# Optimization experiments

Measured on AMD Instinct MI355X. Metric: run time of the kernel, lower is better.

## Reference

```python
import jax, jax.numpy as jnp
import numpy as np

N, NF, D, GH, E, B = 4096, 128, 64, 64, 32768, 32
NG, STEPS = 3, 3  # n_gcn, set2set processing steps


def setup_inputs() -> dict:
    key = jax.random.key(0)
    ks = iter(jax.random.split(key, 64))
    nrm = lambda shape: jax.random.normal(next(ks), shape, dtype=jnp.float32) * 0.05
    inp = {
        'x': jax.random.normal(next(ks), (N, NF), dtype=jnp.float32),
        'edge_attr': jax.random.uniform(next(ks), (E,), dtype=jnp.float32),
        'edge_idx': jax.random.randint(next(ks), (2, E), 0, N),
        'batch_map': jnp.sort(jax.random.randint(next(ks), (N,), 0, B)),
        # pre-GC MLP: NF->D, D->D, D->D (ReLU each)
        'pre_W0': nrm((NF, D)), 'pre_b0': nrm((D,)),
        'pre_W1': nrm((D, D)), 'pre_b1': nrm((D,)),
        'pre_W2': nrm((D, D)), 'pre_b2': nrm((D,)),
        # NNConv edge nets (stacked over NG layers): 1->GH->D*D
        'enn_W1': nrm((NG, 1, GH)), 'enn_b1': nrm((NG, GH)),
        'enn_W2': nrm((NG, GH, D * D)), 'enn_b2': nrm((NG, D * D)),
        'root_W': nrm((NG, D, D)), 'conv_b': nrm((NG, D)),
        # GRU(D, D) per layer, gate order r,z,n (torch), stored transposed for x@W
        'gru_Wih': nrm((NG, D, 3 * D)), 'gru_Whh': nrm((NG, D, 3 * D)),
        'gru_bih': nrm((NG, 3 * D)), 'gru_bhh': nrm((NG, 3 * D)),
        # Set2Set LSTM: input 2D -> hidden D, gate order i,f,g,o (torch)
        's2s_Wih': nrm((2 * D, 4 * D)), 's2s_Whh': nrm((D, 4 * D)),
        's2s_bih': nrm((4 * D,)), 's2s_bhh': nrm((4 * D,)),
        # post-GC MLP: 2D->D, D->D, D->D (ReLU each), then D->1
        'post_W0': nrm((2 * D, D)), 'post_b0': nrm((D,)),
        'post_W1': nrm((D, D)), 'post_b1': nrm((D,)),
        'post_W2': nrm((D, D)), 'post_b2': nrm((D,)),
        'post_W3': nrm((D, 1)), 'post_b3': nrm((1,)),
    }
    return inp


def _forward(x, edge_attr, pre_W0, pre_b0, pre_W1, pre_b1, pre_W2, pre_b2,
             enn_W1, enn_b1, enn_W2, enn_b2, root_W, conv_b,
             gru_Wih, gru_Whh, gru_bih, gru_bhh,
             s2s_Wih, s2s_Whh, s2s_bih, s2s_bhh,
             post_W0, post_b0, post_W1, post_b1, post_W2, post_b2,
             post_W3, post_b3, edge_idx, batch_map):
    relu, sig = jax.nn.relu, jax.nn.sigmoid
    # pre-GC layers
    out = relu(x @ pre_W0 + pre_b0)
    out = relu(out @ pre_W1 + pre_b1)
    out = relu(out @ pre_W2 + pre_b2)  # [N, D]

    src, dst = edge_idx[0], edge_idx[1]
    deg = jax.ops.segment_sum(jnp.ones((E,), out.dtype), dst, num_segments=N)
    deg = jnp.maximum(deg, 1.0)
    ea = edge_attr[:, None]  # view(-1, 1)

    for l in range(NG):
        h = out
        # NNConv: per-edge weight matrix from edge MLP
        We = relu(ea @ enn_W1[l] + enn_b1[l])              # [E, GH]
        We = (We @ enn_W2[l] + enn_b2[l]).reshape(E, D, D)  # [E, D, D]
        msg = jnp.einsum('ei,eio->eo', out[src], We)        # [E, D]
        agg = jax.ops.segment_sum(msg, dst, num_segments=N) / deg[:, None]
        conv = relu(agg + out @ root_W[l] + conv_b[l])
        # single-step GRU update (torch gate order r, z, n)
        gi = conv @ gru_Wih[l] + gru_bih[l]
        gh = h @ gru_Whh[l] + gru_bhh[l]
        i_r, i_z, i_n = jnp.split(gi, 3, axis=-1)
        h_r, h_z, h_n = jnp.split(gh, 3, axis=-1)
        r = sig(i_r + h_r)
        z = sig(i_z + h_z)
        n = jnp.tanh(i_n + r * h_n)
        out = (1.0 - z) * n + z * h

    # Set2Set pooling (early)
    q_star = jnp.zeros((B, 2 * D), out.dtype)
    hh = jnp.zeros((B, D), out.dtype)
    cc = jnp.zeros((B, D), out.dtype)
    for _ in range(STEPS):
        gates = q_star @ s2s_Wih + s2s_bih + hh @ s2s_Whh + s2s_bhh
        gi_, gf, gg, go = jnp.split(gates, 4, axis=-1)
        cc = sig(gf) * cc + sig(gi_) * jnp.tanh(gg)
        hh = sig(go) * jnp.tanh(cc)
        q = hh
        e = jnp.sum(out * q[batch_map], axis=-1)                    # [N]
        m = jax.ops.segment_max(e, batch_map, num_segments=B)
        a = jnp.exp(e - m[batch_map])
        den = jax.ops.segment_sum(a, batch_map, num_segments=B)
        a = a / den[batch_map]
        r_read = jax.ops.segment_sum(a[:, None] * out, batch_map, num_segments=B)
        q_star = jnp.concatenate([q, r_read], axis=-1)              # [B, 2D]

    # post-GC layers
    y = relu(q_star @ post_W0 + post_b0)
    y = relu(y @ post_W1 + post_b1)
    y = relu(y @ post_W2 + post_b2)
    y = y @ post_W3 + post_b3  # [B, 1]
    return y


def reference(x, edge_attr, edge_idx, batch_map, pre_W0, pre_b0, pre_W1, pre_b1,
              pre_W2, pre_b2, enn_W1, enn_b1, enn_W2, enn_b2, root_W, conv_b,
              gru_Wih, gru_Whh, gru_bih, gru_bhh, s2s_Wih, s2s_Whh, s2s_bih,
              s2s_bhh, post_W0, post_b0, post_W1, post_b1, post_W2, post_b2,
              post_W3, post_b3):
    return _forward(x, edge_attr, pre_W0, pre_b0, pre_W1, pre_b1, pre_W2, pre_b2,
                    enn_W1, enn_b1, enn_W2, enn_b2, root_W, conv_b,
                    gru_Wih, gru_Whh, gru_bih, gru_bhh,
                    s2s_Wih, s2s_Whh, s2s_bih, s2s_bhh,
                    post_W0, post_b0, post_W1, post_b1, post_W2, post_b2,
                    post_W3, post_b3, edge_idx, batch_map)
```

## Files before the change

### kernel.cpp

```cpp
#include <hip/hip_runtime.h>
#include <hip/hip_bf16.h>
#include <string.h>

#define NN   4096
#define NE   32768
#define NB   32
#define BKT  64
#define MSG_CHUNK 8

typedef __attribute__((ext_vector_type(8))) short short8;
typedef __attribute__((ext_vector_type(4))) float f4;

__device__ __forceinline__ float sigf(float x) { return 1.0f / (1.0f + __expf(-x)); }
__device__ __forceinline__ short f2bf(float f) {
    __hip_bfloat16 h = __float2bfloat16(f);
    short s;
    memcpy(&s, &h, sizeof(short));
    return s;
}

__global__ __launch_bounds__(256) void k_setup(const float* __restrict__ x,
        const float* __restrict__ W0, const float* __restrict__ b0,
        const float* __restrict__ W1, const float* __restrict__ b1,
        const float* __restrict__ W2, const float* __restrict__ b2,
        const float* __restrict__ enn_W2, __hip_bfloat16* __restrict__ W2F,
        float* __restrict__ out, float* __restrict__ agg,
        int* cnt_src, int* cnt_dst, int* bstart, int* bend) {
    int bid = blockIdx.x, t = threadIdx.x;
    if (bid < 32) {
        int i = bid * 256 + t;
        if (i < NN) cnt_src[i] = 0;
        else cnt_dst[i - NN] = 0;
        if (i < NB) { bstart[i] = 0x7FFFFFFF; bend[i] = 0; }
    } else if (bid < 224) {
        __shared__ __hip_bfloat16 tile[4096];
        size_t base = (size_t)(bid - 32) * 4096;
        for (int i = t; i < 4096; i += 256) {
            int k = i >> 6, o = i & 63;
            int pos = ((o >> 4) << 10) | ((k >> 5) << 9) | (((k >> 3) & 3) << 7)
                    | ((o & 15) << 3) | (k & 7);
            tile[pos] = __float2bfloat16(enn_W2[base + i]);
        }
        __syncthreads();
        for (int i = t; i < 4096; i += 256) W2F[base + i] = tile[i];
    } else {
        __shared__ float xr[4][128], ha[4][64], hb[4][64];
        int w = t >> 6, j = t & 63;
        int n = (bid - 224) * 4 + w;
        xr[w][j] = x[(size_t)n * 128 + j];
        xr[w][64 + j] = x[(size_t)n * 128 + 64 + j];
        agg[(size_t)n * 64 + j] = 0.f;
        float s = b0[j];
        #pragma unroll 8
        for (int k = 0; k < 128; ++k) s = fmaf(xr[w][k], W0[k * 64 + j], s);
        ha[w][j] = fmaxf(s, 0.f);
        s = b1[j];
        #pragma unroll 8
        for (int k = 0; k < 64; ++k) s = fmaf(ha[w][k], W1[k * 64 + j], s);
        hb[w][j] = fmaxf(s, 0.f);
        s = b2[j];
        #pragma unroll 8
        for (int k = 0; k < 64; ++k) s = fmaf(hb[w][k], W2[k * 64 + j], s);
        out[(size_t)n * 64 + j] = fmaxf(s, 0.f);
    }
}

__global__ __launch_bounds__(256) void k_bucket(const int* __restrict__ eidx,
        const float* __restrict__ ea, const int* __restrict__ bm,
        const float* __restrict__ Wih, const float* __restrict__ Whh,
        float* __restrict__ WihT, float* __restrict__ WhhT,
        int* cnt_src, int* cnt_dst, int* csr_dst, float* csr_ea,
        int* bstart, int* bend) {
    int t = threadIdx.x;
    if (blockIdx.x >= 128) {
        int c0 = (blockIdx.x - 128) * 8;
        for (int i = t; i < 1024; i += 256) {
            int c = c0 + (i >> 7), j = i & 127;
            WihT[(size_t)c * 128 + j] = Wih[(size_t)j * 256 + c];
        }
        for (int i = t; i < 512; i += 256) {
            int c = c0 + (i >> 6), j = i & 63;
            WhhT[(size_t)c * 64 + j] = Whh[(size_t)j * 256 + c];
        }
        return;
    }
    int e = blockIdx.x * 256 + t;
    if (e < NE) {
        int s = eidx[e];
        int d = eidx[NE + e];
        int slot = atomicAdd(&cnt_src[s], 1);
        if (slot < BKT) {
            csr_dst[s * BKT + slot] = d;
            csr_ea[s * BKT + slot] = ea[e];
        }
        atomicAdd(&cnt_dst[d], 1);
    }
    if (e < NN) {
        int b = bm[e];
        atomicMin(&bstart[b], e);
        atomicMax(&bend[b], e + 1);
    }
}

__global__ __launch_bounds__(256, 2) void k_fused(const float* __restrict__ out,
        const __hip_bfloat16* __restrict__ W2F_l, const float* __restrict__ b2l,
        const float* __restrict__ W1l, const float* __restrict__ b1l,
        const int* __restrict__ cnt_src, const int* __restrict__ csr_dst,
        const float* __restrict__ csr_ea, float* __restrict__ agg) {
    __shared__ __hip_bfloat16 Pt[8 * 4096];
    __shared__ float outs[8][68];
    __shared__ float wlds[4][MSG_CHUNK][64];
    int t = threadIdx.x, wave = t >> 6, lane = t & 63;
    int laneM = lane & 15, quad = lane >> 4;
    int n0 = blockIdx.x * 8;
    for (int i = t; i < 512; i += 256) outs[i >> 6][i & 63] = out[(size_t)n0 * 64 + i];
    __syncthreads();
    short8 a0, a1;
    {
        const float* ar = &outs[laneM & 7][quad * 8];
        #pragma unroll
        for (int j = 0; j < 8; ++j) a0[j] = f2bf(ar[j]);
        const float* ar2 = &outs[laneM & 7][32 + quad * 8];
        #pragma unroll
        for (int j = 0; j < 8; ++j) a1[j] = f2bf(ar2[j]);
    }
    float btr[2] = {0.f, 0.f};
    for (int k = 0; k < 64; ++k) {
        float bv = b2l[k * 64 + lane];
        #pragma unroll
        for (int u = 0; u < 2; ++u) btr[u] = fmaf(outs[wave * 2 + u][k], bv, btr[u]);
    }
    #pragma unroll 2
    for (int gp = 0; gp < 8; ++gp) {
        int gA = wave * 16 + gp * 2;
        const __hip_bfloat16* BgA = W2F_l + (size_t)gA * 4096;
        const __hip_bfloat16* BgB = BgA + 4096;
        int c = gA >> 3;
        int p = (gA >> 1) & 3;
        char* wb = (char*)Pt + (quad << 15) + (c << 10) + (laneM << 4)
                 + (((p ^ quad) & 3) << 2);
        #pragma unroll
        for (int sub = 0; sub < 4; ++sub) {
            short8 bA0 = *(const short8*)(BgA + sub * 1024 + lane * 8);
            short8 bA1 = *(const short8*)(BgA + sub * 1024 + 512 + lane * 8);
            short8 bB0 = *(const short8*)(BgB + sub * 1024 + lane * 8);
            short8 bB1 = *(const short8*)(BgB + sub * 1024 + 512 + lane * 8);
            f4 accA = {0.f, 0.f, 0.f, 0.f}, accB = {0.f, 0.f, 0.f, 0.f};
            accA = __builtin_amdgcn_mfma_f32_16x16x32_bf16(a0, bA0, accA, 0, 0, 0);
            accA = __builtin_amdgcn_mfma_f32_16x16x32_bf16(a1, bA1, accA, 0, 0, 0);
            accB = __builtin_amdgcn_mfma_f32_16x16x32_bf16(a0, bB0, accB, 0, 0, 0);
            accB = __builtin_amdgcn_mfma_f32_16x16x32_bf16(a1, bB1, accB, 0, 0, 0);
            if (quad < 2) {
                char* wbs = wb + (sub << 8);
                #pragma unroll
                for (int r = 0; r < 4; ++r) {
                    unsigned pk = (unsigned)(unsigned short)f2bf(accA[r])
                                | ((unsigned)(unsigned short)f2bf(accB[r]) << 16);
                    *(unsigned*)(wbs + (r << 13)) = pk;
                }
            }
        }
    }
    __syncthreads();
    float w1v = W1l[lane], b1v = b1l[lane];
    for (int u = 0; u < 2; ++u) {
        int nloc = wave * 2 + u;
        int n = n0 + nloc;
        int deg = cnt_src[n];
        if (deg > BKT) deg = BKT;
        if (deg <= 0) continue;
        int wq = nloc >> 2;
        float preg[64];
        const char* Pn = (const char*)Pt + (nloc << 13);
        #pragma unroll
        for (int c = 0; c < 8; ++c) {
            uint4 vv = *(const uint4*)(Pn + (c << 10) + (lane << 4));
            unsigned d0 = vv.x, d1 = vv.y, d2 = vv.z, d3 = vv.w;
            if (wq & 1) { unsigned tt = d0; d0 = d1; d1 = tt; tt = d2; d2 = d3; d3 = tt; }
            union { unsigned u2; float f; } cv;
            cv.u2 = d0 << 16;          preg[c * 8 + 0] = cv.f;
            cv.u2 = d0 & 0xFFFF0000u;  preg[c * 8 + 1] = cv.f;
            cv.u2 = d1 << 16;          preg[c * 8 + 2] = cv.f;
            cv.u2 = d1 & 0xFFFF0000u;  preg[c * 8 + 3] = cv.f;
            cv.u2 = d2 << 16;          preg[c * 8 + 4] = cv.f;
            cv.u2 = d2 & 0xFFFF0000u;  preg[c * 8 + 5] = cv.f;
            cv.u2 = d3 << 16;          preg[c * 8 + 6] = cv.f;
            cv.u2 = d3 & 0xFFFF0000u;  preg[c * 8 + 7] = cv.f;
        }
        float bt = btr[u];
        const int* bdst = csr_dst + n * BKT;
        const float* bea = csr_ea + n * BKT;
        for (int c0 = 0; c0 < deg; c0 += MSG_CHUNK) {
            int cc = deg - c0;
            if (cc > MSG_CHUNK) cc = MSG_CHUNK;
            int dl = 0; float el = 0.f;
            if (lane < cc) { dl = bdst[c0 + lane]; el = bea[c0 + lane]; }
            for (int si = 0; si < cc; ++si) {
                float eav = __shfl(el, si, 64);
                wlds[wave][si][lane] = fmaxf(fmaf(eav, w1v, b1v), 0.f);
            }
            for (int i = 0; i < cc; ++i) {
                int dst = __shfl(dl, i, 64);
                const float* wr = wlds[wave][i];
                float acc0 = bt, acc1 = 0.f, acc2 = 0.f, acc3 = 0.f;
                #pragma unroll
                for (int g = 0; g < 64; g += 16) {
                    float4 w0 = *(const float4*)(wr + g);
                    float4 w1 = *(const float4*)(wr + g + 4);
                    float4 w2 = *(const float4*)(wr + g + 8);
                    float4 w3 = *(const float4*)(wr + g + 12);
                    acc0 = fmaf(w0.x, preg[g], acc0);
                    acc0 = fmaf(w0.y, preg[g + 1], acc0);
                    acc0 = fmaf(w0.z, preg[g + 2], acc0);
                    acc0 = fmaf(w0.w, preg[g + 3], acc0);
                    acc1 = fmaf(w1.x, preg[g + 4], acc1);
                    acc1 = fmaf(w1.y, preg[g + 5], acc1);
                    acc1 = fmaf(w1.z, preg[g + 6], acc1);
                    acc1 = fmaf(w1.w, preg[g + 7], acc1);
                    acc2 = fmaf(w2.x, preg[g + 8], acc2);
                    acc2 = fmaf(w2.y, preg[g + 9], acc2);
                    acc2 = fmaf(w2.z, preg[g + 10], acc2);
                    acc2 = fmaf(w2.w, preg[g + 11], acc2);
                    acc3 = fmaf(w3.x, preg[g + 12], acc3);
                    acc3 = fmaf(w3.y, preg[g + 13], acc3);
                    acc3 = fmaf(w3.z, preg[g + 14], acc3);
                    acc3 = fmaf(w3.w, preg[g + 15], acc3);
                }
                float acc = (acc0 + acc1) + (acc2 + acc3);
                atomicAdd(&agg[(size_t)dst * 64 + lane], acc);
            }
        }
    }
}

__global__ __launch_bounds__(256) void k_gru(const float* __restrict__ out,
        float* __restrict__ agg, const int* __restrict__ cnt_dst,
        const float* __restrict__ rootW, const float* __restrict__ convb,
        const float* __restrict__ Wih, const float* __restrict__ Whh,
        const float* __restrict__ bih, const float* __restrict__ bhh,
        float* __restrict__ outn) {
    __shared__ float sh[4][64], sc[4][64];
    int t = threadIdx.x, w = t >> 6, j = t & 63;
    int n = blockIdx.x * 4 + w;
    float hj = out[(size_t)n * 64 + j];
    sh[w][j] = hj;
    int dg = cnt_dst[n];
    float invd = 1.0f / (float)(dg > 0 ? dg : 1);
    float av = agg[(size_t)n * 64 + j];
    agg[(size_t)n * 64 + j] = 0.f;
    __syncthreads();
    float s = av * invd + convb[j];
    #pragma unroll 8
    for (int k = 0; k < 64; ++k) s = fmaf(sh[w][k], rootW[k * 64 + j], s);
    float conv = fmaxf(s, 0.f);
    sc[w][j] = conv;
    __syncthreads();
    float gir = bih[j], giz = bih[64 + j], gin = bih[128 + j];
    float ghr = bhh[j], ghz = bhh[64 + j], ghn = bhh[128 + j];
    #pragma unroll 4
    for (int k = 0; k < 64; ++k) {
        float c = sc[w][k], h = sh[w][k];
        gir = fmaf(c, Wih[k * 192 + j], gir);
        giz = fmaf(c, Wih[k * 192 + 64 + j], giz);
        gin = fmaf(c, Wih[k * 192 + 128 + j], gin);
        ghr = fmaf(h, Whh[k * 192 + j], ghr);
        ghz = fmaf(h, Whh[k * 192 + 64 + j], ghz);
        ghn = fmaf(h, Whh[k * 192 + 128 + j], ghn);
    }
    float r = sigf(gir + ghr);
    float z = sigf(giz + ghz);
    float nn = tanhf(gin + r * ghn);
    outn[(size_t)n * 64 + j] = (1.f - z) * nn + z * hj;
}

__global__ __launch_bounds__(256, 1) void k_s2s_post(const float* __restrict__ out,
        const int* __restrict__ bstart, const int* __restrict__ bend,
        const float* __restrict__ WihT, const float* __restrict__ WhhT,
        const float* __restrict__ bih, const float* __restrict__ bhh,
        const float* __restrict__ pW0, const float* __restrict__ pb0,
        const float* __restrict__ pW1, const float* __restrict__ pb1,
        const float* __restrict__ pW2, const float* __restrict__ pb2,
        const float* __restrict__ pW3, const float* __restrict__ pb3,
        float* __restrict__ y) {
    __shared__ float cacheT[64 * 193];
    __shared__ float wpost[16448];
    __shared__ float qs[128];
    __shared__ float hh_l[64];
    __shared__ float gates_l[256];
    __shared__ float ebuf[1024];
    __shared__ float redw[4], redw2[4];
    __shared__ float redbuf[4][64];
    __shared__ float tmp64[64];
    int t = threadIdx.x, wave = t >> 6, lane = t & 63;
    int b = blockIdx.x;
    int s0 = bstart[b], e0 = bend[b];
    int cnt = e0 - s0;
    if (cnt < 0) cnt = 0;
    if (cnt > 1024) cnt = 1024;
    int ccnt = cnt < 192 ? cnt : 192;
    int nf4 = ccnt * 16;
    const float4* out4 = (const float4*)(out + (size_t)s0 * 64);
    float4 stg[12];
    #pragma unroll
    for (int i = 0; i < 12; ++i) {
        int v = t + i * 256;
        if (v < nf4) stg[i] = out4[v];
    }
    #pragma unroll
    for (int i = 0; i < 12; ++i) {
        int v = t + i * 256;
        if (v < nf4) {
            int row = v >> 4, dq = v & 15;
            cacheT[(dq * 4 + 0) * 193 + row] = stg[i].x;
            cacheT[(dq * 4 + 1) * 193 + row] = stg[i].y;
            cacheT[(dq * 4 + 2) * 193 + row] = stg[i].z;
            cacheT[(dq * 4 + 3) * 193 + row] = stg[i].w;
        }
    }
    {
        float4* wp4 = (float4*)wpost;
        #pragma unroll
        for (int i = 0; i < 8; ++i) {
            int v = t + i * 256;
            wp4[v] = ((const float4*)pW0)[v];
        }
        #pragma unroll
        for (int i = 0; i < 4; ++i) {
            int v = t + i * 256;
            wp4[2048 + v] = ((const float4*)pW1)[v];
        }
        #pragma unroll
        for (int i = 0; i < 4; ++i) {
            int v = t + i * 256;
            wp4[3072 + v] = ((const float4*)pW2)[v];
        }
        if (t < 16) wp4[4096 + t] = ((const float4*)pW3)[t];
    }
    const float4* wihT4 = (const float4*)(WihT + (size_t)t * 128);
    const float4* whhT4 = (const float4*)(WhhT + (size_t)t * 64);
    float bsum = bih[t] + bhh[t];
    float ccr = 0.f;
    if (t < 128) qs[t] = 0.f;
    if (t < 64) hh_l[t] = 0.f;
    __syncthreads();
    const float4* qs4 = (const float4*)qs;
    const float4* hh4 = (const float4*)hh_l;
    for (int step = 0; step < 3; ++step) {
        float g0 = bsum, g1 = 0.f, g2 = 0.f, g3 = 0.f;
        #pragma unroll
        for (int jq = 0; jq < 32; ++jq) {
            float4 w = wihT4[jq];
            float4 v = qs4[jq];
            g0 = fmaf(v.x, w.x, g0);
            g1 = fmaf(v.y, w.y, g1);
            g2 = fmaf(v.z, w.z, g2);
            g3 = fmaf(v.w, w.w, g3);
        }
        #pragma unroll
        for (int jq = 0; jq < 16; ++jq) {
            float4 w = whhT4[jq];
            float4 v = hh4[jq];
            g0 = fmaf(v.x, w.x, g0);
            g1 = fmaf(v.y, w.y, g1);
            g2 = fmaf(v.z, w.z, g2);
            g3 = fmaf(v.w, w.w, g3);
        }
        gates_l[t] = (g0 + g1) + (g2 + g3);
        __syncthreads();
        if (t < 64) {
            float cn = sigf(gates_l[64 + t]) * ccr
                     + sigf(gates_l[t]) * tanhf(gates_l[128 + t]);
            ccr = cn;
            hh_l[t] = sigf(gates_l[192 + t]) * tanhf(cn);
        }
        __syncthreads();
        for (int idx = t; idx < cnt; idx += 256) {
            float s0a = 0.f, s1a = 0.f, s2a = 0.f, s3a = 0.f;
            if (idx < 192) {
                #pragma unroll
                for (int dq = 0; dq < 16; ++dq) {
                    float4 h = hh4[dq];
                    s0a = fmaf(cacheT[(dq * 4 + 0) * 193 + idx], h.x, s0a);
                    s1a = fmaf(cacheT[(dq * 4 + 1) * 193 + idx], h.y, s1a);
                    s2a = fmaf(cacheT[(dq * 4 + 2) * 193 + idx], h.z, s2a);
                    s3a = fmaf(cacheT[(dq * 4 + 3) * 193 + idx], h.w, s3a);
                }
            } else {
                const float* row = out + (size_t)(s0 + idx) * 64;
                #pragma unroll
                for (int dq = 0; dq < 16; ++dq) {
                    float4 h = hh4[dq];
                    s0a = fmaf(row[dq * 4 + 0], h.x, s0a);
                    s1a = fmaf(row[dq * 4 + 1], h.y, s1a);
                    s2a = fmaf(row[dq * 4 + 2], h.z, s2a);
                    s3a = fmaf(row[dq * 4 + 3], h.w, s3a);
                }
            }
            ebuf[idx] = (s0a + s1a) + (s2a + s3a);
        }
        __syncthreads();
        float lm = -3.0e38f;
        for (int idx = t; idx < cnt; idx += 256) lm = fmaxf(lm, ebuf[idx]);
        #pragma unroll
        for (int off = 32; off > 0; off >>= 1) lm = fmaxf(lm, __shfl_xor(lm, off, 64));
        if (lane == 0) redw[wave] = lm;
        __syncthreads();
        float m = fmaxf(fmaxf(redw[0], redw[1]), fmaxf(redw[2], redw[3]));
        float ls = 0.f;
        for (int idx = t; idx < cnt; idx += 256) {
            float a = __expf(ebuf[idx] - m);
            ebuf[idx] = a;
            ls += a;
        }
        #pragma unroll
        for (int off = 32; off > 0; off >>= 1) ls += __shfl_xor(ls, off, 64);
        if (lane == 0) redw2[wave] = ls;
        __syncthreads();
        float ssum = (redw2[0] + redw2[1]) + (redw2[2] + redw2[3]);
        float inv = (cnt > 0) ? 1.f / ssum : 0.f;
        float r0 = 0.f;
        for (int row = wave; row < ccnt; row += 4)
            r0 = fmaf(ebuf[row], cacheT[lane * 193 + row], r0);
        for (int row = 192 + wave; row < cnt; row += 4)
            r0 = fmaf(ebuf[row], out[(size_t)(s0 + row) * 64 + lane], r0);
        redbuf[wave][lane] = r0;
        __syncthreads();
        if (t < 64) {
            float s = ((redbuf[0][t] + redbuf[1][t]) + (redbuf[2][t] + redbuf[3][t]));
            qs[64 + t] = s * inv;
            qs[t] = hh_l[t];
        }
        __syncthreads();
    }
    if (t < 64) {
        float s = pb0[t];
        #pragma unroll 4
        for (int k = 0; k < 128; ++k) s = fmaf(qs[k], wpost[k * 64 + t], s);
        tmp64[t] = fmaxf(s, 0.f);
    }
    __syncthreads();
    float h1v = 0.f;
    if (t < 64) {
        float s = pb1[t];
        #pragma unroll 4
        for (int k = 0; k < 64; ++k) s = fmaf(tmp64[k], wpost[8192 + k * 64 + t], s);
        h1v = fmaxf(s, 0.f);
    }
    __syncthreads();
    if (t < 64) tmp64[t] = h1v;
    __syncthreads();
    if (t < 64) {
        float s = pb2[t];
        #pragma unroll 4
        for (int k = 0; k < 64; ++k) s = fmaf(tmp64[k], wpost[12288 + k * 64 + t], s);
        gates_l[t] = fmaxf(s, 0.f) * wpost[16384 + t];
    }
    __syncthreads();
    if (t == 0) {
        float yy = pb3[0];
        for (int k = 0; k < 64; ++k) yy += gates_l[k];
        y[b] = yy;
    }
}


extern "C" void kernel_launch(void* const* d_in, const int* in_sizes, int n_in,
                              void* d_out, int out_size, void* d_ws, size_t ws_size,
                              hipStream_t stream) {
    const float* x         = (const float*)d_in[0];
    const float* edge_attr = (const float*)d_in[1];
    const int*   edge_idx  = (const int*)d_in[2];
    const int*   batch_map = (const int*)d_in[3];
    const float* pre_W0 = (const float*)d_in[4];
    const float* pre_b0 = (const float*)d_in[5];
    const float* pre_W1 = (const float*)d_in[6];
    const float* pre_b1 = (const float*)d_in[7];
    const float* pre_W2 = (const float*)d_in[8];
    const float* pre_b2 = (const float*)d_in[9];
    const float* enn_W1 = (const float*)d_in[10];
    const float* enn_b1 = (const float*)d_in[11];
    const float* enn_W2 = (const float*)d_in[12];
    const float* enn_b2 = (const float*)d_in[13];
    const float* root_W = (const float*)d_in[14];
    const float* conv_b = (const float*)d_in[15];
    const float* gru_Wih = (const float*)d_in[16];
    const float* gru_Whh = (const float*)d_in[17];
    const float* gru_bih = (const float*)d_in[18];
    const float* gru_bhh = (const float*)d_in[19];
    const float* s2s_Wih = (const float*)d_in[20];
    const float* s2s_Whh = (const float*)d_in[21];
    const float* s2s_bih = (const float*)d_in[22];
    const float* s2s_bhh = (const float*)d_in[23];
    const float* post_W0 = (const float*)d_in[24];
    const float* post_b0 = (const float*)d_in[25];
    const float* post_W1 = (const float*)d_in[26];
    const float* post_b1 = (const float*)d_in[27];
    const float* post_W2 = (const float*)d_in[28];
    const float* post_b2 = (const float*)d_in[29];
    const float* post_W3 = (const float*)d_in[30];
    const float* post_b3 = (const float*)d_in[31];
    float* yout = (float*)d_out;

    char* wp = (char*)d_ws;
    auto take = [&](size_t bytes) -> char* {
        char* r = wp;
        wp += (bytes + 255) & ~(size_t)255;
        return r;
    };
    float* outA = (float*)take((size_t)NN * 64 * 4);
    float* outB = (float*)take((size_t)NN * 64 * 4);
    float* agg  = (float*)take((size_t)NN * 64 * 4);
    __hip_bfloat16* W2F = (__hip_bfloat16*)take((size_t)3 * 64 * 4096 * 2);
    int* cnt_src  = (int*)take((size_t)NN * 4);
    int* cnt_dst  = (int*)take((size_t)NN * 4);
    int* csr_dst  = (int*)take((size_t)NN * BKT * 4);
    float* csr_ea = (float*)take((size_t)NN * BKT * 4);
    int* bstart   = (int*)take((size_t)NB * 4);
    int* bend     = (int*)take((size_t)NB * 4);
    float* WihT   = (float*)take((size_t)256 * 128 * 4);
    float* WhhT   = (float*)take((size_t)256 * 64 * 4);

    k_setup<<<1248, 256, 0, stream>>>(x, pre_W0, pre_b0, pre_W1, pre_b1, pre_W2, pre_b2,
                                      enn_W2, W2F, outA, agg, cnt_src, cnt_dst,
                                      bstart, bend);
    k_bucket<<<160, 256, 0, stream>>>(edge_idx, edge_attr, batch_map,
                                      s2s_Wih, s2s_Whh, WihT, WhhT,
                                      cnt_src, cnt_dst, csr_dst, csr_ea, bstart, bend);

    float* cur = outA;
    float* nxt = outB;
    for (int l = 0; l < 3; ++l) {
        k_fused<<<NN / 8, 256, 0, stream>>>(cur, W2F + (size_t)l * 64 * 4096,
                                            enn_b2 + (size_t)l * 4096,
                                            enn_W1 + l * 64, enn_b1 + l * 64,
                                            cnt_src, csr_dst, csr_ea, agg);
        k_gru<<<NN / 4, 256, 0, stream>>>(cur, agg, cnt_dst, root_W + l * 4096,
                                          conv_b + l * 64, gru_Wih + l * 64 * 192,
                                          gru_Whh + l * 64 * 192, gru_bih + l * 192,
                                          gru_bhh + l * 192, nxt);
        float* tmp = cur; cur = nxt; nxt = tmp;
    }
    k_s2s_post<<<NB, 256, 0, stream>>>(cur, bstart, bend, WihT, WhhT, s2s_bih,
                                       s2s_bhh, post_W0, post_b0, post_W1, post_b1,
                                       post_W2, post_b2, post_W3, post_b3, yout);
}
```

Baseline: 348.8 us.

## Fuse pre-MLP, NNConv message passing and GRU layers into one cooperative kernel

Replaces the per-layer k_fused/k_gru launches and the pre-MLP stage with a single cooperative persistent kernel of 512 blocks. Each block keeps its 8 node states in shared memory across all three layers and uses grid.sync between the scatter and GRU phases. This removes six kernel launches and the global round-trips of node features between layers. The cost is grid-wide barriers, a requirement that all 512 blocks be co-resident, and atomicExch to read and reset the aggregate buffer.

```diff
diff --git a/kernel.cpp b/kernel.cpp
--- a/kernel.cpp
+++ b/kernel.cpp
@@ -1,6 +1,9 @@
 #include <hip/hip_runtime.h>
 #include <hip/hip_bf16.h>
+#include <hip/hip_cooperative_groups.h>
 #include <string.h>
+
+namespace cg = cooperative_groups;
 
 #define NN   4096
 #define NE   32768
@@ -19,12 +22,8 @@
     return s;
 }
 
-__global__ __launch_bounds__(256) void k_setup(const float* __restrict__ x,
-        const float* __restrict__ W0, const float* __restrict__ b0,
-        const float* __restrict__ W1, const float* __restrict__ b1,
-        const float* __restrict__ W2, const float* __restrict__ b2,
-        const float* __restrict__ enn_W2, __hip_bfloat16* __restrict__ W2F,
-        float* __restrict__ out, float* __restrict__ agg,
+__global__ __launch_bounds__(256) void k_setup(const float* __restrict__ enn_W2,
+        __hip_bfloat16* __restrict__ W2F, float* __restrict__ agg,
         int* cnt_src, int* cnt_dst, int* bstart, int* bend) {
     int bid = blockIdx.x, t = threadIdx.x;
     if (bid < 32) {
@@ -32,7 +31,8 @@
         if (i < NN) cnt_src[i] = 0;
         else cnt_dst[i - NN] = 0;
         if (i < NB) { bstart[i] = 0x7FFFFFFF; bend[i] = 0; }
-    } else if (bid < 224) {
+        for (int z = i; z < NN * 64; z += 8192) agg[z] = 0.f;
+    } else {
         __shared__ __hip_bfloat16 tile[4096];
         size_t base = (size_t)(bid - 32) * 4096;
         for (int i = t; i < 4096; i += 256) {
@@ -43,25 +43,6 @@
         }
         __syncthreads();
         for (int i = t; i < 4096; i += 256) W2F[base + i] = tile[i];
-    } else {
-        __shared__ float xr[4][128], ha[4][64], hb[4][64];
-        int w = t >> 6, j = t & 63;
-        int n = (bid - 224) * 4 + w;
-        xr[w][j] = x[(size_t)n * 128 + j];
-        xr[w][64 + j] = x[(size_t)n * 128 + 64 + j];
-        agg[(size_t)n * 64 + j] = 0.f;
-        float s = b0[j];
-        #pragma unroll 8
-        for (int k = 0; k < 128; ++k) s = fmaf(xr[w][k], W0[k * 64 + j], s);
-        ha[w][j] = fmaxf(s, 0.f);
-        s = b1[j];
-        #pragma unroll 8
-        for (int k = 0; k < 64; ++k) s = fmaf(ha[w][k], W1[k * 64 + j], s);
-        hb[w][j] = fmaxf(s, 0.f);
-        s = b2[j];
-        #pragma unroll 8
-        for (int k = 0; k < 64; ++k) s = fmaf(hb[w][k], W2[k * 64 + j], s);
-        out[(size_t)n * 64 + j] = fmaxf(s, 0.f);
     }
 }
 
@@ -102,175 +83,218 @@
     }
 }
 
-__global__ __launch_bounds__(256, 2) void k_fused(const float* __restrict__ out,
-        const __hip_bfloat16* __restrict__ W2F_l, const float* __restrict__ b2l,
-        const float* __restrict__ W1l, const float* __restrict__ b1l,
-        const int* __restrict__ cnt_src, const int* __restrict__ csr_dst,
-        const float* __restrict__ csr_ea, float* __restrict__ agg) {
+__global__ __launch_bounds__(256, 2) void k_mega(const float* __restrict__ x,
+        const float* __restrict__ mW0, const float* __restrict__ mb0,
+        const float* __restrict__ mW1, const float* __restrict__ mb1,
+        const float* __restrict__ mW2, const float* __restrict__ mb2,
+        const __hip_bfloat16* __restrict__ W2F, const float* __restrict__ enn_b2,
+        const float* __restrict__ enn_W1, const float* __restrict__ enn_b1,
+        const float* __restrict__ rootW, const float* __restrict__ convb,
+        const float* __restrict__ gWih, const float* __restrict__ gWhh,
+        const float* __restrict__ gbih, const float* __restrict__ gbhh,
+        const int* __restrict__ cnt_src, const int* __restrict__ cnt_dst,
+        const int* __restrict__ csr_dst, const float* __restrict__ csr_ea,
+        float* __restrict__ agg, float* __restrict__ outG) {
+    cg::grid_group grid = cg::this_grid();
+    __shared__ float outs[8][68];
     __shared__ __hip_bfloat16 Pt[8 * 4096];
-    __shared__ float outs[8][68];
     __shared__ float wlds[4][MSG_CHUNK][64];
     int t = threadIdx.x, wave = t >> 6, lane = t & 63;
     int laneM = lane & 15, quad = lane >> 4;
     int n0 = blockIdx.x * 8;
-    for (int i = t; i < 512; i += 256) outs[i >> 6][i & 63] = out[(size_t)n0 * 64 + i];
-    __syncthreads();
-    short8 a0, a1;
-    {
-        const float* ar = &outs[laneM & 7][quad * 8];
-        #pragma unroll
-        for (int j = 0; j < 8; ++j) a0[j] = f2bf(ar[j]);
-        const float* ar2 = &outs[laneM & 7][32 + quad * 8];
-        #pragma unroll
-        for (int j = 0; j < 8; ++j) a1[j] = f2bf(ar2[j]);
-    }
-    float btr[2] = {0.f, 0.f};
-    for (int k = 0; k < 64; ++k) {
-        float bv = b2l[k * 64 + lane];
-        #pragma unroll
-        for (int u = 0; u < 2; ++u) btr[u] = fmaf(outs[wave * 2 + u][k], bv, btr[u]);
-    }
-    #pragma unroll 2
-    for (int gp = 0; gp < 8; ++gp) {
-        int gA = wave * 16 + gp * 2;
-        const __hip_bfloat16* BgA = W2F_l + (size_t)gA * 4096;
-        const __hip_bfloat16* BgB = BgA + 4096;
-        int c = gA >> 3;
-        int p = (gA >> 1) & 3;
-        char* wb = (char*)Pt + (quad << 15) + (c << 10) + (laneM << 4)
-                 + (((p ^ quad) & 3) << 2);
-        #pragma unroll
-        for (int sub = 0; sub < 4; ++sub) {
-            short8 bA0 = *(const short8*)(BgA + sub * 1024 + lane * 8);
-            short8 bA1 = *(const short8*)(BgA + sub * 1024 + 512 + lane * 8);
-            short8 bB0 = *(const short8*)(BgB + sub * 1024 + lane * 8);
-            short8 bB1 = *(const short8*)(BgB + sub * 1024 + 512 + lane * 8);
-            f4 accA = {0.f, 0.f, 0.f, 0.f}, accB = {0.f, 0.f, 0.f, 0.f};
-            accA = __builtin_amdgcn_mfma_f32_16x16x32_bf16(a0, bA0, accA, 0, 0, 0);
-            accA = __builtin_amdgcn_mfma_f32_16x16x32_bf16(a1, bA1, accA, 0, 0, 0);
-            accB = __builtin_amdgcn_mfma_f32_16x16x32_bf16(a0, bB0, accB, 0, 0, 0);
-            accB = __builtin_amdgcn_mfma_f32_16x16x32_bf16(a1, bB1, accB, 0, 0, 0);
-            if (quad < 2) {
-                char* wbs = wb + (sub << 8);
-                #pragma unroll
-                for (int r = 0; r < 4; ++r) {
-                    unsigned pk = (unsigned)(unsigned short)f2bf(accA[r])
-                                | ((unsigned)(unsigned short)f2bf(accB[r]) << 16);
-                    *(unsigned*)(wbs + (r << 13)) = pk;
+    int j = lane;
+    float* xs  = (float*)Pt;
+    float* haL = &wlds[0][0][0];
+    float* hbL = haL + 512;
+    for (int i = t; i < 1024; i += 256) xs[i] = x[(size_t)n0 * 128 + i];
+    __syncthreads();
+    for (int u = 0; u < 2; ++u) {
+        int nl = wave * 2 + u;
+        const float* xr = xs + nl * 128;
+        float s = mb0[j];
+        #pragma unroll 8
+        for (int k = 0; k < 128; ++k) s = fmaf(xr[k], mW0[k * 64 + j], s);
+        haL[nl * 64 + j] = fmaxf(s, 0.f);
+        s = mb1[j];
+        #pragma unroll 8
+        for (int k = 0; k < 64; ++k) s = fmaf(haL[nl * 64 + k], mW1[k * 64 + j], s);
+        hbL[nl * 64 + j] = fmaxf(s, 0.f);
+        s = mb2[j];
+        #pragma unroll 8
+        for (int k = 0; k < 64; ++k) s = fmaf(hbL[nl * 64 + k], mW2[k * 64 + j], s);
+        outs[nl][j] = fmaxf(s, 0.f);
+    }
+    __syncthreads();
+    for (int l = 0; l < 3; ++l) {
+        const __hip_bfloat16* W2F_l = W2F + (size_t)l * 64 * 4096;
+        const float* b2l = enn_b2 + (size_t)l * 4096;
+        const float* W1l = enn_W1 + l * 64;
+        const float* b1l = enn_b1 + l * 64;
+        short8 a0, a1;
+        {
+            const float* ar = &outs[laneM & 7][quad * 8];
+            #pragma unroll
+            for (int q = 0; q < 8; ++q) a0[q] = f2bf(ar[q]);
+            const float* ar2 = &outs[laneM & 7][32 + quad * 8];
+            #pragma unroll
+            for (int q = 0; q < 8; ++q) a1[q] = f2bf(ar2[q]);
+        }
+        float btr[2] = {0.f, 0.f};
+        for (int k = 0; k < 64; ++k) {
+            float bv = b2l[k * 64 + lane];
+            #pragma unroll
+            for (int u = 0; u < 2; ++u) btr[u] = fmaf(outs[wave * 2 + u][k], bv, btr[u]);
+        }
+        #pragma unroll 2
+        for (int gp = 0; gp < 8; ++gp) {
+            int gA = wave * 16 + gp * 2;
+            const __hip_bfloat16* BgA = W2F_l + (size_t)gA * 4096;
+            const __hip_bfloat16* BgB = BgA + 4096;
+            int c = gA >> 3;
+            int p = (gA >> 1) & 3;
+            char* wb = (char*)Pt + (quad << 15) + (c << 10) + (laneM << 4)
+                     + (((p ^ quad) & 3) << 2);
+            #pragma unroll
+            for (int sub = 0; sub < 4; ++sub) {
+                short8 bA0 = *(const short8*)(BgA + sub * 1024 + lane * 8);
+                short8 bA1 = *(const short8*)(BgA + sub * 1024 + 512 + lane * 8);
+                short8 bB0 = *(const short8*)(BgB + sub * 1024 + lane * 8);
+                short8 bB1 = *(const short8*)(BgB + sub * 1024 + 512 + lane * 8);
+                f4 accA = {0.f, 0.f, 0.f, 0.f}, accB = {0.f, 0.f, 0.f, 0.f};
+                accA = __builtin_amdgcn_mfma_f32_16x16x32_bf16(a0, bA0, accA, 0, 0, 0);
+                accA = __builtin_amdgcn_mfma_f32_16x16x32_bf16(a1, bA1, accA, 0, 0, 0);
+                accB = __builtin_amdgcn_mfma_f32_16x16x32_bf16(a0, bB0, accB, 0, 0, 0);
+                accB = __builtin_amdgcn_mfma_f32_16x16x32_bf16(a1, bB1, accB, 0, 0, 0);
+                if (quad < 2) {
+                    char* wbs = wb + (sub << 8);
+                    #pragma unroll
+                    for (int r = 0; r < 4; ++r) {
+                        unsigned pk = (unsigned)(unsigned short)f2bf(accA[r])
+                                    | ((unsigned)(unsigned short)f2bf(accB[r]) << 16);
+                        *(unsigned*)(wbs + (r << 13)) = pk;
+                    }
                 }
             }
         }
-    }
-    __syncthreads();
-    float w1v = W1l[lane], b1v = b1l[lane];
-    for (int u = 0; u < 2; ++u) {
-        int nloc = wave * 2 + u;
-        int n = n0 + nloc;
-        int deg = cnt_src[n];
-        if (deg > BKT) deg = BKT;
-        if (deg <= 0) continue;
-        int wq = nloc >> 2;
-        float preg[64];
-        const char* Pn = (const char*)Pt + (nloc << 13);
-        #pragma unroll
-        for (int c = 0; c < 8; ++c) {
-            uint4 vv = *(const uint4*)(Pn + (c << 10) + (lane << 4));
-            unsigned d0 = vv.x, d1 = vv.y, d2 = vv.z, d3 = vv.w;
-            if (wq & 1) { unsigned tt = d0; d0 = d1; d1 = tt; tt = d2; d2 = d3; d3 = tt; }
-            union { unsigned u2; float f; } cv;
-            cv.u2 = d0 << 16;          preg[c * 8 + 0] = cv.f;
-            cv.u2 = d0 & 0xFFFF0000u;  preg[c * 8 + 1] = cv.f;
-            cv.u2 = d1 << 16;          preg[c * 8 + 2] = cv.f;
-            cv.u2 = d1 & 0xFFFF0000u;  preg[c * 8 + 3] = cv.f;
-            cv.u2 = d2 << 16;          preg[c * 8 + 4] = cv.f;
-            cv.u2 = d2 & 0xFFFF0000u;  preg[c * 8 + 5] = cv.f;
-            cv.u2 = d3 << 16;          preg[c * 8 + 6] = cv.f;
-            cv.u2 = d3 & 0xFFFF0000u;  preg[c * 8 + 7] = cv.f;
-        }
-        float bt = btr[u];
-        const int* bdst = csr_dst + n * BKT;
-        const float* bea = csr_ea + n * BKT;
-        for (int c0 = 0; c0 < deg; c0 += MSG_CHUNK) {
-            int cc = deg - c0;
-            if (cc > MSG_CHUNK) cc = MSG_CHUNK;
-            int dl = 0; float el = 0.f;
-            if (lane < cc) { dl = bdst[c0 + lane]; el = bea[c0 + lane]; }
-            for (int si = 0; si < cc; ++si) {
-                float eav = __shfl(el, si, 64);
-                wlds[wave][si][lane] = fmaxf(fmaf(eav, w1v, b1v), 0.f);
+        __syncthreads();
+        float w1v = W1l[lane], b1v = b1l[lane];
+        for (int u = 0; u < 2; ++u) {
+            int nloc = wave * 2 + u;
+            int n = n0 + nloc;
+            int deg = cnt_src[n];
+            if (deg > BKT) deg = BKT;
+            if (deg <= 0) continue;
+            int wq = nloc >> 2;
+            float preg[64];
+            const char* Pn = (const char*)Pt + (nloc << 13);
+            #pragma unroll
+            for (int c = 0; c < 8; ++c) {
+                uint4 vv = *(const uint4*)(Pn + (c << 10) + (lane << 4));
+                unsigned d0 = vv.x, d1 = vv.y, d2 = vv.z, d3 = vv.w;
+                if (wq & 1) { unsigned tt = d0; d0 = d1; d1 = tt; tt = d2; d2 = d3; d3 = tt; }
+                union { unsigned u2; float f; } cv;
+                cv.u2 = d0 << 16;          preg[c * 8 + 0] = cv.f;
+                cv.u2 = d0 & 0xFFFF0000u;  preg[c * 8 + 1] = cv.f;
+                cv.u2 = d1 << 16;          preg[c * 8 + 2] = cv.f;
+                cv.u2 = d1 & 0xFFFF0000u;  preg[c * 8 + 3] = cv.f;
+                cv.u2 = d2 << 16;          preg[c * 8 + 4] = cv.f;
+                cv.u2 = d2 & 0xFFFF0000u;  preg[c * 8 + 5] = cv.f;
+                cv.u2 = d3 << 16;          preg[c * 8 + 6] = cv.f;
+                cv.u2 = d3 & 0xFFFF0000u;  preg[c * 8 + 7] = cv.f;
             }
-            for (int i = 0; i < cc; ++i) {
-                int dst = __shfl(dl, i, 64);
-                const float* wr = wlds[wave][i];
-                float acc0 = bt, acc1 = 0.f, acc2 = 0.f, acc3 = 0.f;
-                #pragma unroll
-                for (int g = 0; g < 64; g += 16) {
-                    float4 w0 = *(const float4*)(wr + g);
-                    float4 w1 = *(const float4*)(wr + g + 4);
-                    float4 w2 = *(const float4*)(wr + g + 8);
-                    float4 w3 = *(const float4*)(wr + g + 12);
-                    acc0 = fmaf(w0.x, preg[g], acc0);
-                    acc0 = fmaf(w0.y, preg[g + 1], acc0);
-                    acc0 = fmaf(w0.z, preg[g + 2], acc0);
-                    acc0 = fmaf(w0.w, preg[g + 3], acc0);
-                    acc1 = fmaf(w1.x, preg[g + 4], acc1);
-                    acc1 = fmaf(w1.y, preg[g + 5], acc1);
-                    acc1 = fmaf(w1.z, preg[g + 6], acc1);
-                    acc1 = fmaf(w1.w, preg[g + 7], acc1);
-                    acc2 = fmaf(w2.x, preg[g + 8], acc2);
-                    acc2 = fmaf(w2.y, preg[g + 9], acc2);
-                    acc2 = fmaf(w2.z, preg[g + 10], acc2);
-                    acc2 = fmaf(w2.w, preg[g + 11], acc2);
-                    acc3 = fmaf(w3.x, preg[g + 12], acc3);
-                    acc3 = fmaf(w3.y, preg[g + 13], acc3);
-                    acc3 = fmaf(w3.z, preg[g + 14], acc3);
-                    acc3 = fmaf(w3.w, preg[g + 15], acc3);
+            float bt = btr[u];
+            const int* bdst = csr_dst + n * BKT;
+            const float* bea = csr_ea + n * BKT;
+            for (int c0 = 0; c0 < deg; c0 += MSG_CHUNK) {
+                int cc = deg - c0;
+                if (cc > MSG_CHUNK) cc = MSG_CHUNK;
+                int dl = 0; float el = 0.f;
+                if (lane < cc) { dl = bdst[c0 + lane]; el = bea[c0 + lane]; }
+                for (int si = 0; si < cc; ++si) {
+                    float eav = __shfl(el, si, 64);
+                    wlds[wave][si][lane] = fmaxf(fmaf(eav, w1v, b1v), 0.f);
                 }
-                float acc = (acc0 + acc1) + (acc2 + acc3);
-                atomicAdd(&agg[(size_t)dst * 64 + lane], acc);
+                for (int i = 0; i < cc; ++i) {
+                    int dst = __shfl(dl, i, 64);
+                    const float* wr = wlds[wave][i];
+                    float acc0 = bt, acc1 = 0.f, acc2 = 0.f, acc3 = 0.f;
+                    #pragma unroll
+                    for (int g = 0; g < 64; g += 16) {
+                        float4 w0 = *(const float4*)(wr + g);
+                        float4 w1 = *(const float4*)(wr + g + 4);
+                        float4 w2 = *(const float4*)(wr + g + 8);
+                        float4 w3 = *(const float4*)(wr + g + 12);
+                        acc0 = fmaf(w0.x, preg[g], acc0);
+                        acc0 = fmaf(w0.y, preg[g + 1], acc0);
+                        acc0 = fmaf(w0.z, preg[g + 2], acc0);
+                        acc0 = fmaf(w0.w, preg[g + 3], acc0);
+                        acc1 = fmaf(w1.x, preg[g + 4], acc1);
+                        acc1 = fmaf(w1.y, preg[g + 5], acc1);
+                        acc1 = fmaf(w1.z, preg[g + 6], acc1);
+                        acc1 = fmaf(w1.w, preg[g + 7], acc1);
+                        acc2 = fmaf(w2.x, preg[g + 8], acc2);
+                        acc2 = fmaf(w2.y, preg[g + 9], acc2);
+                        acc2 = fmaf(w2.z, preg[g + 10], acc2);
+                        acc2 = fmaf(w2.w, preg[g + 11], acc2);
+                        acc3 = fmaf(w3.x, preg[g + 12], acc3);
+                        acc3 = fmaf(w3.y, preg[g + 13], acc3);
+                        acc3 = fmaf(w3.z, preg[g + 14], acc3);
+                        acc3 = fmaf(w3.w, preg[g + 15], acc3);
+                    }
+                    float acc = (acc0 + acc1) + (acc2 + acc3);
+                    atomicAdd(&agg[(size_t)dst * 64 + lane], acc);
+                }
             }
         }
-    }
-}
-
-__global__ __launch_bounds__(256) void k_gru(const float* __restrict__ out,
-        float* __restrict__ agg, const int* __restrict__ cnt_dst,
-        const float* __restrict__ rootW, const float* __restrict__ convb,
-        const float* __restrict__ Wih, const float* __restrict__ Whh,
-        const float* __restrict__ bih, const float* __restrict__ bhh,
-        float* __restrict__ outn) {
-    __shared__ float sh[4][64], sc[4][64];
-    int t = threadIdx.x, w = t >> 6, j = t & 63;
-    int n = blockIdx.x * 4 + w;
-    float hj = out[(size_t)n * 64 + j];
-    sh[w][j] = hj;
-    int dg = cnt_dst[n];
-    float invd = 1.0f / (float)(dg > 0 ? dg : 1);
-    float av = agg[(size_t)n * 64 + j];
-    agg[(size_t)n * 64 + j] = 0.f;
-    __syncthreads();
-    float s = av * invd + convb[j];
-    #pragma unroll 8
-    for (int k = 0; k < 64; ++k) s = fmaf(sh[w][k], rootW[k * 64 + j], s);
-    float conv = fmaxf(s, 0.f);
-    sc[w][j] = conv;
-    __syncthreads();
-    float gir = bih[j], giz = bih[64 + j], gin = bih[128 + j];
-    float ghr = bhh[j], ghz = bhh[64 + j], ghn = bhh[128 + j];
-    #pragma unroll 4
-    for (int k = 0; k < 64; ++k) {
-        float c = sc[w][k], h = sh[w][k];
-        gir = fmaf(c, Wih[k * 192 + j], gir);
-        giz = fmaf(c, Wih[k * 192 + 64 + j], giz);
-        gin = fmaf(c, Wih[k * 192 + 128 + j], gin);
-        ghr = fmaf(h, Whh[k * 192 + j], ghr);
-        ghz = fmaf(h, Whh[k * 192 + 64 + j], ghz);
-        ghn = fmaf(h, Whh[k * 192 + 128 + j], ghn);
-    }
-    float r = sigf(gir + ghr);
-    float z = sigf(giz + ghz);
-    float nn = tanhf(gin + r * ghn);
-    outn[(size_t)n * 64 + j] = (1.f - z) * nn + z * hj;
+        __threadfence();
+        grid.sync();
+        const float* rootWl = rootW + (size_t)l * 4096;
+        const float* convbl = convb + l * 64;
+        const float* Wihl = gWih + (size_t)l * 64 * 192;
+        const float* Whhl = gWhh + (size_t)l * 64 * 192;
+        const float* bihl = gbih + l * 192;
+        const float* bhhl = gbhh + l * 192;
+        float* scL = haL;
+        for (int u = 0; u < 2; ++u) {
+            int nl = wave * 2 + u;
+            int n = n0 + nl;
+            int dg = cnt_dst[n];
+            float invd = 1.0f / (float)(dg > 0 ? dg : 1);
+            float av = atomicExch(&agg[(size_t)n * 64 + j], 0.f);
+            float s = av * invd + convbl[j];
+            #pragma unroll 8
+            for (int k = 0; k < 64; ++k) s = fmaf(outs[nl][k], rootWl[k * 64 + j], s);
+            scL[nl * 64 + j] = fmaxf(s, 0.f);
+        }
+        __syncthreads();
+        float o_new[2];
+        for (int u = 0; u < 2; ++u) {
+            int nl = wave * 2 + u;
+            float hj = outs[nl][j];
+            float gir = bihl[j], giz = bihl[64 + j], gin = bihl[128 + j];
+            float ghr = bhhl[j], ghz = bhhl[64 + j], ghn = bhhl[128 + j];
+            #pragma unroll 4
+            for (int k = 0; k < 64; ++k) {
+                float c = scL[nl * 64 + k], h = outs[nl][k];
+                gir = fmaf(c, Wihl[k * 192 + j], gir);
+                giz = fmaf(c, Wihl[k * 192 + 64 + j], giz);
+                gin = fmaf(c, Wihl[k * 192 + 128 + j], gin);
+                ghr = fmaf(h, Whhl[k * 192 + j], ghr);
+                ghz = fmaf(h, Whhl[k * 192 + 64 + j], ghz);
+                ghn = fmaf(h, Whhl[k * 192 + 128 + j], ghn);
+            }
+            float r = sigf(gir + ghr);
+            float z = sigf(giz + ghz);
+            float nn2 = tanhf(gin + r * ghn);
+            o_new[u] = (1.f - z) * nn2 + z * hj;
+        }
+        __syncthreads();
+        for (int u = 0; u < 2; ++u) outs[wave * 2 + u][j] = o_new[u];
+        __threadfence();
+        grid.sync();
+    }
+    for (int i = t; i < 512; i += 256)
+        outG[(size_t)n0 * 64 + i] = outs[i >> 6][i & 63];
 }
 
 __global__ __launch_bounds__(256, 1) void k_s2s_post(const float* __restrict__ out,
@@ -508,7 +532,6 @@
         return r;
     };
     float* outA = (float*)take((size_t)NN * 64 * 4);
-    float* outB = (float*)take((size_t)NN * 64 * 4);
     float* agg  = (float*)take((size_t)NN * 64 * 4);
     __hip_bfloat16* W2F = (__hip_bfloat16*)take((size_t)3 * 64 * 4096 * 2);
     int* cnt_src  = (int*)take((size_t)NN * 4);
@@ -520,27 +543,22 @@
     float* WihT   = (float*)take((size_t)256 * 128 * 4);
     float* WhhT   = (float*)take((size_t)256 * 64 * 4);
 
-    k_setup<<<1248, 256, 0, stream>>>(x, pre_W0, pre_b0, pre_W1, pre_b1, pre_W2, pre_b2,
-                                      enn_W2, W2F, outA, agg, cnt_src, cnt_dst,
-                                      bstart, bend);
+    k_setup<<<224, 256, 0, stream>>>(enn_W2, W2F, agg, cnt_src, cnt_dst, bstart, bend);
     k_bucket<<<160, 256, 0, stream>>>(edge_idx, edge_attr, batch_map,
                                       s2s_Wih, s2s_Whh, WihT, WhhT,
                                       cnt_src, cnt_dst, csr_dst, csr_ea, bstart, bend);
 
-    float* cur = outA;
-    float* nxt = outB;
-    for (int l = 0; l < 3; ++l) {
-        k_fused<<<NN / 8, 256, 0, stream>>>(cur, W2F + (size_t)l * 64 * 4096,
-                                            enn_b2 + (size_t)l * 4096,
-                                            enn_W1 + l * 64, enn_b1 + l * 64,
-                                            cnt_src, csr_dst, csr_ea, agg);
-        k_gru<<<NN / 4, 256, 0, stream>>>(cur, agg, cnt_dst, root_W + l * 4096,
-                                          conv_b + l * 64, gru_Wih + l * 64 * 192,
-                                          gru_Whh + l * 64 * 192, gru_bih + l * 192,
-                                          gru_bhh + l * 192, nxt);
-        float* tmp = cur; cur = nxt; nxt = tmp;
-    }
-    k_s2s_post<<<NB, 256, 0, stream>>>(cur, bstart, bend, WihT, WhhT, s2s_bih,
+    void* margs[] = { (void*)&x,
+        (void*)&pre_W0, (void*)&pre_b0, (void*)&pre_W1, (void*)&pre_b1,
+        (void*)&pre_W2, (void*)&pre_b2,
+        (void*)&W2F, (void*)&enn_b2, (void*)&enn_W1, (void*)&enn_b1,
+        (void*)&root_W, (void*)&conv_b,
+        (void*)&gru_Wih, (void*)&gru_Whh, (void*)&gru_bih, (void*)&gru_bhh,
+        (void*)&cnt_src, (void*)&cnt_dst, (void*)&csr_dst, (void*)&csr_ea,
+        (void*)&agg, (void*)&outA };
+    hipLaunchCooperativeKernel((void*)k_mega, dim3(512), dim3(256), margs, 0, stream);
+
+    k_s2s_post<<<NB, 256, 0, stream>>>(outA, bstart, bend, WihT, WhhT, s2s_bih,
                                        s2s_bhh, post_W0, post_b0, post_W1, post_b1,
                                        post_W2, post_b2, post_W3, post_b3, yout);
 }
```

New measurement: 938.2 us. 2.69x slower.

## Split fused edge-message kernel across two hidden-channel halves per node tile

Applied to the files above, without the earlier changes.

Each 8-node tile is now processed by two blocks, each covering half of the 64 edge-net hidden channels. This halves shared memory for the projected weights and the per-node register array, and the launch bound is raised to allow 4 blocks per CU. The aim is more occupancy and more blocks in flight for this latency-bound edge loop. The cost is that each edge's destination accumulation is now done twice as partial sums, doubling atomic adds to agg, and half the lanes sit idle when writing the edge-net activations.

```diff
diff --git a/kernel.cpp b/kernel.cpp
--- a/kernel.cpp
+++ b/kernel.cpp
@@ -102,17 +102,18 @@
     }
 }
 
-__global__ __launch_bounds__(256, 2) void k_fused(const float* __restrict__ out,
+__global__ __launch_bounds__(256, 4) void k_fused(const float* __restrict__ out,
         const __hip_bfloat16* __restrict__ W2F_l, const float* __restrict__ b2l,
         const float* __restrict__ W1l, const float* __restrict__ b1l,
         const int* __restrict__ cnt_src, const int* __restrict__ csr_dst,
         const float* __restrict__ csr_ea, float* __restrict__ agg) {
-    __shared__ __hip_bfloat16 Pt[8 * 4096];
+    __shared__ __hip_bfloat16 Pt[8 * 2048];
     __shared__ float outs[8][68];
-    __shared__ float wlds[4][MSG_CHUNK][64];
+    __shared__ float wlds[4][MSG_CHUNK][32];
     int t = threadIdx.x, wave = t >> 6, lane = t & 63;
     int laneM = lane & 15, quad = lane >> 4;
-    int n0 = blockIdx.x * 8;
+    int ntile = blockIdx.x >> 1, gc = blockIdx.x & 1;
+    int n0 = ntile * 8;
     for (int i = t; i < 512; i += 256) outs[i >> 6][i & 63] = out[(size_t)n0 * 64 + i];
     __syncthreads();
     short8 a0, a1;
@@ -125,19 +126,22 @@
         for (int j = 0; j < 8; ++j) a1[j] = f2bf(ar2[j]);
     }
     float btr[2] = {0.f, 0.f};
-    for (int k = 0; k < 64; ++k) {
-        float bv = b2l[k * 64 + lane];
-        #pragma unroll
-        for (int u = 0; u < 2; ++u) btr[u] = fmaf(outs[wave * 2 + u][k], bv, btr[u]);
-    }
-    #pragma unroll 2
-    for (int gp = 0; gp < 8; ++gp) {
-        int gA = wave * 16 + gp * 2;
+    if (gc == 0) {
+        for (int k = 0; k < 64; ++k) {
+            float bv = b2l[k * 64 + lane];
+            #pragma unroll
+            for (int u = 0; u < 2; ++u) btr[u] = fmaf(outs[wave * 2 + u][k], bv, btr[u]);
+        }
+    }
+    #pragma unroll
+    for (int gp = 0; gp < 4; ++gp) {
+        int glA = wave * 8 + gp * 2;
+        int gA = gc * 32 + glA;
         const __hip_bfloat16* BgA = W2F_l + (size_t)gA * 4096;
         const __hip_bfloat16* BgB = BgA + 4096;
-        int c = gA >> 3;
-        int p = (gA >> 1) & 3;
-        char* wb = (char*)Pt + (quad << 15) + (c << 10) + (laneM << 4)
+        int c = wave;
+        int p = gp;
+        char* wb = (char*)Pt + (quad << 14) + (c << 10) + (laneM << 4)
                  + (((p ^ quad) & 3) << 2);
         #pragma unroll
         for (int sub = 0; sub < 4; ++sub) {
@@ -156,13 +160,14 @@
                 for (int r = 0; r < 4; ++r) {
                     unsigned pk = (unsigned)(unsigned short)f2bf(accA[r])
                                 | ((unsigned)(unsigned short)f2bf(accB[r]) << 16);
-                    *(unsigned*)(wbs + (r << 13)) = pk;
+                    *(unsigned*)(wbs + (r << 12)) = pk;
                 }
             }
         }
     }
     __syncthreads();
-    float w1v = W1l[lane], b1v = b1l[lane];
+    float w1v = (lane < 32) ? W1l[gc * 32 + lane] : 0.f;
+    float b1v = (lane < 32) ? b1l[gc * 32 + lane] : 0.f;
     for (int u = 0; u < 2; ++u) {
         int nloc = wave * 2 + u;
         int n = n0 + nloc;
@@ -170,22 +175,22 @@
         if (deg > BKT) deg = BKT;
         if (deg <= 0) continue;
         int wq = nloc >> 2;
-        float preg[64];
-        const char* Pn = (const char*)Pt + (nloc << 13);
-        #pragma unroll
-        for (int c = 0; c < 8; ++c) {
-            uint4 vv = *(const uint4*)(Pn + (c << 10) + (lane << 4));
+        float preg[32];
+        const char* Pn = (const char*)Pt + (nloc << 12);
+        #pragma unroll
+        for (int c2 = 0; c2 < 4; ++c2) {
+            uint4 vv = *(const uint4*)(Pn + (c2 << 10) + (lane << 4));
             unsigned d0 = vv.x, d1 = vv.y, d2 = vv.z, d3 = vv.w;
             if (wq & 1) { unsigned tt = d0; d0 = d1; d1 = tt; tt = d2; d2 = d3; d3 = tt; }
             union { unsigned u2; float f; } cv;
-            cv.u2 = d0 << 16;          preg[c * 8 + 0] = cv.f;
-            cv.u2 = d0 & 0xFFFF0000u;  preg[c * 8 + 1] = cv.f;
-            cv.u2 = d1 << 16;          preg[c * 8 + 2] = cv.f;
-            cv.u2 = d1 & 0xFFFF0000u;  preg[c * 8 + 3] = cv.f;
-            cv.u2 = d2 << 16;          preg[c * 8 + 4] = cv.f;
-            cv.u2 = d2 & 0xFFFF0000u;  preg[c * 8 + 5] = cv.f;
-            cv.u2 = d3 << 16;          preg[c * 8 + 6] = cv.f;
-            cv.u2 = d3 & 0xFFFF0000u;  preg[c * 8 + 7] = cv.f;
+            cv.u2 = d0 << 16;          preg[c2 * 8 + 0] = cv.f;
+            cv.u2 = d0 & 0xFFFF0000u;  preg[c2 * 8 + 1] = cv.f;
+            cv.u2 = d1 << 16;          preg[c2 * 8 + 2] = cv.f;
+            cv.u2 = d1 & 0xFFFF0000u;  preg[c2 * 8 + 3] = cv.f;
+            cv.u2 = d2 << 16;          preg[c2 * 8 + 4] = cv.f;
+            cv.u2 = d2 & 0xFFFF0000u;  preg[c2 * 8 + 5] = cv.f;
+            cv.u2 = d3 << 16;          preg[c2 * 8 + 6] = cv.f;
+            cv.u2 = d3 & 0xFFFF0000u;  preg[c2 * 8 + 7] = cv.f;
         }
         float bt = btr[u];
         const int* bdst = csr_dst + n * BKT;
@@ -197,14 +202,15 @@
             if (lane < cc) { dl = bdst[c0 + lane]; el = bea[c0 + lane]; }
             for (int si = 0; si < cc; ++si) {
                 float eav = __shfl(el, si, 64);
-                wlds[wave][si][lane] = fmaxf(fmaf(eav, w1v, b1v), 0.f);
+                if (lane < 32)
+                    wlds[wave][si][lane] = fmaxf(fmaf(eav, w1v, b1v), 0.f);
             }
             for (int i = 0; i < cc; ++i) {
                 int dst = __shfl(dl, i, 64);
                 const float* wr = wlds[wave][i];
                 float acc0 = bt, acc1 = 0.f, acc2 = 0.f, acc3 = 0.f;
                 #pragma unroll
-                for (int g = 0; g < 64; g += 16) {
+                for (int g = 0; g < 32; g += 16) {
                     float4 w0 = *(const float4*)(wr + g);
                     float4 w1 = *(const float4*)(wr + g + 4);
                     float4 w2 = *(const float4*)(wr + g + 8);
@@ -320,20 +326,11 @@
     {
         float4* wp4 = (float4*)wpost;
         #pragma unroll
-        for (int i = 0; i < 8; ++i) {
-            int v = t + i * 256;
-            wp4[v] = ((const float4*)pW0)[v];
-        }
-        #pragma unroll
-        for (int i = 0; i < 4; ++i) {
-            int v = t + i * 256;
-            wp4[2048 + v] = ((const float4*)pW1)[v];
-        }
-        #pragma unroll
-        for (int i = 0; i < 4; ++i) {
-            int v = t + i * 256;
-            wp4[3072 + v] = ((const float4*)pW2)[v];
-        }
+        for (int i = 0; i < 8; ++i) { int v = t + i * 256; wp4[v] = ((const float4*)pW0)[v]; }
+        #pragma unroll
+        for (int i = 0; i < 4; ++i) { int v = t + i * 256; wp4[2048 + v] = ((const float4*)pW1)[v]; }
+        #pragma unroll
+        for (int i = 0; i < 4; ++i) { int v = t + i * 256; wp4[3072 + v] = ((const float4*)pW2)[v]; }
         if (t < 16) wp4[4096 + t] = ((const float4*)pW3)[t];
     }
     const float4* wihT4 = (const float4*)(WihT + (size_t)t * 128);
@@ -530,10 +527,10 @@
     float* cur = outA;
     float* nxt = outB;
     for (int l = 0; l < 3; ++l) {
-        k_fused<<<NN / 8, 256, 0, stream>>>(cur, W2F + (size_t)l * 64 * 4096,
-                                            enn_b2 + (size_t)l * 4096,
-                                            enn_W1 + l * 64, enn_b1 + l * 64,
-                                            cnt_src, csr_dst, csr_ea, agg);
+        k_fused<<<NN / 8 * 2, 256, 0, stream>>>(cur, W2F + (size_t)l * 64 * 4096,
+                                                enn_b2 + (size_t)l * 4096,
+                                                enn_W1 + l * 64, enn_b1 + l * 64,
+                                                cnt_src, csr_dst, csr_ea, agg);
         k_gru<<<NN / 4, 256, 0, stream>>>(cur, agg, cnt_dst, root_W + l * 4096,
                                           conv_b + l * 64, gru_Wih + l * 64 * 192,
                                           gru_Whh + l * 64 * 192, gru_bih + l * 192,
```

After: 329.6 us. 5.5% less time.
